# Optimization experiments

Hardware: AMD Instinct MI355X
Metric: run time of the kernel (lower is better)

The kernel has to match this reference:

```python
import jax, jax.numpy as jnp
import numpy as np

B, S, D = 4, 2048, 1024
H, DK, DV = 16, 64, 64
SCALE = 8.0  # scaling_factor = sqrt(dk)


def setup_inputs() -> dict:
    key = jax.random.key(0)
    ks = jax.random.split(key, 9)
    s = 1.0 / np.sqrt(D)
    return {
        "q": jax.random.normal(ks[0], (B, S, D), jnp.float32),
        "k": jax.random.normal(ks[1], (B, S, D), jnp.float32),
        "v": jax.random.normal(ks[2], (B, S, D), jnp.float32),
        "Wq": jax.random.uniform(ks[3], (D, H * DK), jnp.float32, -s, s),
        "bq": jax.random.uniform(ks[4], (H * DK,), jnp.float32, -s, s),
        "Wk": jax.random.uniform(ks[5], (D, H * DK), jnp.float32, -s, s),
        "bk": jax.random.uniform(ks[6], (H * DK,), jnp.float32, -s, s),
        "Wv": jax.random.uniform(ks[7], (D, H * DV), jnp.float32, -s, s),
        "bv": jax.random.uniform(ks[8], (H * DV,), jnp.float32, -s, s),
    }


def reference(q, k, v, Wq, bq, Wk, bk, Wv, bv):
    # Linear projections, then split heads: [B,S,H*d] -> [B,S,H,d]
    qh = (q @ Wq + bq).reshape(B, S, H, DK)
    kh = (k @ Wk + bk).reshape(B, S, H, DK)
    vh = (v @ Wv + bv).reshape(B, S, H, DV)
    # scores: [B,H,Sq,Sk]
    e = jnp.einsum("bqhd,bkhd->bhqk", qh, kh) / SCALE
    attn = jax.nn.softmax(e, axis=-1)
    out = jnp.einsum("bhqk,bkhd->bqhd", attn, vh)  # [B,Sq,H,DV]
    return out.reshape(B, S, H * DV)  # dropout p=0 -> identity
```

## Files before the change

### kernel.cpp

```cpp
#include <hip/hip_runtime.h>
#include <hip/hip_bf16.h>


typedef unsigned short u16;
typedef unsigned int   u32;
typedef short bf16x8 __attribute__((ext_vector_type(8)));
typedef short bf16x4 __attribute__((ext_vector_type(4)));
typedef float f32x4  __attribute__((ext_vector_type(4)));
typedef u32   u32x4  __attribute__((ext_vector_type(4)));

#define S_TOT 2048
#define HD    1024
#define QK_SCALE 0.18033688f

#if __has_builtin(__builtin_amdgcn_exp2f)
#define EXP2(x) __builtin_amdgcn_exp2f(x)
#else
#define EXP2(x) exp2f(x)
#endif

__device__ __forceinline__ u16 f2bf(float f) {
  union { float f; unsigned u; } v; v.f = f;
  unsigned r = v.u + 0x7FFFu + ((v.u >> 16) & 1u);
  return (u16)(r >> 16);
}

__device__ __forceinline__ u32 cvt_pk_bf16(float lo, float hi) {
  u32 r;
  asm("v_cvt_pk_bf16_f32 %0, %1, %2" : "=v"(r) : "v"(lo), "v"(hi));
  return r;
}

__device__ __forceinline__ bf16x4 ds_tr16(unsigned a) {
  bf16x4 d;
  asm volatile("ds_read_b64_tr_b16 %0, %1" : "=v"(d) : "v"(a) : "memory");
  return d;
}

__device__ __forceinline__ void gld16(const u16* g, u16* l) {
  __builtin_amdgcn_global_load_lds(
      (const __attribute__((address_space(1))) u32*)g,
      (__attribute__((address_space(3))) u32*)l, 16, 0, 0);
}

#define LGKM_FENCE() do { asm volatile("s_waitcnt lgkmcnt(0)" ::: "memory"); \
                          __builtin_amdgcn_sched_barrier(0); } while (0)

__global__ __launch_bounds__(256)
void conv_kernel(const float* __restrict__ x0, const float* __restrict__ x1, const float* __restrict__ x2,
                 const float* __restrict__ w0, const float* __restrict__ w1, const float* __restrict__ w2,
                 u16* __restrict__ Xb, u16* __restrict__ Wt)
{
  const int z = blockIdx.y;
  const int t = threadIdx.x;
  if (blockIdx.x < 1024) {
    const float* X = z == 0 ? x0 : (z == 1 ? x1 : x2);
    u16* Xz = Xb + (size_t)z * 8388608;
    int tid = blockIdx.x * 256 + t;
#pragma unroll
    for (int i = 0; i < 8; ++i) {
      int c = tid + i * 262144;
      int row = c >> 8, k4 = (c & 255) * 4;
      const float4 xv = *(const float4*)&X[(size_t)row * 1024 + k4];
      int p = (k4 & ~31) + 8 * ((k4 & 15) >> 2) + 4 * ((k4 >> 4) & 1);
      bf16x4 sv = { (short)f2bf(xv.x), (short)f2bf(xv.y), (short)f2bf(xv.z), (short)f2bf(xv.w) };
      *(bf16x4*)&Xz[(size_t)row * 1024 + p] = sv;
    }
  } else {
    const float* W = z == 0 ? w0 : (z == 1 ? w1 : w2);
    u16* Wz = Wt + (size_t)z * 1048576;
    int tid = (blockIdx.x - 1024) * 256 + t;
#pragma unroll
    for (int i = 0; i < 8; ++i) {
      int c = tid + i * 32768;
      int k = c >> 8, n4 = (c & 255) * 4;
      const float4 wv = *(const float4*)&W[(size_t)k * 1024 + n4];
      int off = ((n4 >> 7) * 32 + (k >> 5)) * 4096 + ((n4 >> 4) & 7) * 512
              + ((k >> 4) & 1) * 256 + (k & 15) * 16 + (n4 & 15);
      bf16x4 sv = { (short)f2bf(wv.x), (short)f2bf(wv.y), (short)f2bf(wv.z), (short)f2bf(wv.w) };
      *(bf16x4*)&Wz[off] = sv;
    }
  }
}

__global__ __launch_bounds__(256)
void gemm_kernel(const u16* __restrict__ Xb, const u16* __restrict__ Wt,
                 const float* __restrict__ b0, const float* __restrict__ b1, const float* __restrict__ b2,
                 u16* __restrict__ o0, u16* __restrict__ o1, u16* __restrict__ vT)
{
  int p  = blockIdx.x + 8 * blockIdx.y + 512 * blockIdx.z;
  int wk = (p & 7) * 192 + (p >> 3);
  int nb = wk & 7, mb = (wk >> 3) & 63, z = wk >> 9;

  const u16* Xz = Xb + (size_t)z * 8388608;
  const u16* Wz = Wt + (size_t)z * 1048576;
  const float* BS = z == 0 ? b0 : (z == 1 ? b1 : b2);
  const float  osc = (z == 0) ? QK_SCALE : 1.0f;

  const int t = threadIdx.x;
  const int lane = t & 63, wid = t >> 6;
  const int g = lane >> 4, ln = lane & 15;
  const int mbase = mb * 128, nbase = nb * 128;

  __shared__ __align__(16) u16 Al[128 * 32];
  __shared__ __align__(16) u16 Bl[16 * 256];

  f32x4 acc[4][4];
#pragma unroll
  for (int i = 0; i < 4; ++i)
#pragma unroll
    for (int j = 0; j < 4; ++j) { acc[i][j][0]=0.f; acc[i][j][1]=0.f; acc[i][j][2]=0.f; acc[i][j][3]=0.f; }

  const u16* sa = Xz + (size_t)(mbase + (t >> 2)) * 1024 + (t & 3) * 8;
  const u16* sb = Wz + (size_t)(nb * 32) * 4096 + t * 8;
  u16* al_w = &Al[wid * 512];
  u16* bl_w = &Bl[wid * 512];

  if (z < 2) {
    const int wm = wid >> 1, wn = wid & 1;
    u16* O = z == 0 ? o0 : o1;
    const unsigned bs_base = (unsigned)(size_t)&Bl[0] + (unsigned)((wn * 4) * 1024) + lane * 8;

    for (int kb = 0; kb < 32; ++kb) {
      gld16(sa + kb * 32,                 al_w);
      gld16(sa + kb * 32 + 64 * 1024,     al_w + 2048);
      gld16(sb + kb * 4096,               bl_w);
      gld16(sb + kb * 4096 + 2048,        bl_w + 2048);
      __syncthreads();

      bf16x8 af[4];
#pragma unroll
      for (int mf = 0; mf < 4; ++mf)
        af[mf] = *(const bf16x8*)&Al[(wm * 64 + mf * 16 + ln) * 32 + g * 8];

      bf16x8 bfv[4];
#pragma unroll
      for (int nf = 0; nf < 4; ++nf) {
        bf16x4 lo = ds_tr16(bs_base + (unsigned)(nf * 1024));
        bf16x4 hi = ds_tr16(bs_base + (unsigned)(nf * 1024 + 512));
        bf16x8 bb;
        bb[0]=lo[0]; bb[1]=lo[1]; bb[2]=lo[2]; bb[3]=lo[3];
        bb[4]=hi[0]; bb[5]=hi[1]; bb[6]=hi[2]; bb[7]=hi[3];
        bfv[nf] = bb;
      }
      LGKM_FENCE();
#pragma unroll
      for (int mf = 0; mf < 4; ++mf)
#pragma unroll
        for (int nf = 0; nf < 4; ++nf)
          acc[mf][nf] = __builtin_amdgcn_mfma_f32_16x16x32_bf16(af[mf], bfv[nf], acc[mf][nf], 0, 0, 0);
      __syncthreads();
    }

#pragma unroll
    for (int nf = 0; nf < 4; ++nf) {
      int n = nbase + wn * 64 + nf * 16 + ln;
      float bv = BS[n];
#pragma unroll
      for (int mf = 0; mf < 4; ++mf)
#pragma unroll
        for (int r = 0; r < 4; ++r) {
          int m = mbase + wm * 64 + mf * 16 + 4 * g + r;
          O[(size_t)m * 1024 + n] = f2bf((acc[mf][nf][r] + bv) * osc);
        }
    }
  } else {
    const int wseq = wid >> 1, wdv = wid & 1;
    const unsigned bs_base2 = (unsigned)(size_t)&Bl[0] + (unsigned)((wdv * 4) * 1024) + lane * 8;

    for (int kb = 0; kb < 32; ++kb) {
      gld16(sa + kb * 32,                 al_w);
      gld16(sa + kb * 32 + 64 * 1024,     al_w + 2048);
      gld16(sb + kb * 4096,               bl_w);
      gld16(sb + kb * 4096 + 2048,        bl_w + 2048);
      __syncthreads();

      bf16x8 afw[4];
#pragma unroll
      for (int mf = 0; mf < 4; ++mf) {
        bf16x4 lo = ds_tr16(bs_base2 + (unsigned)(mf * 1024));
        bf16x4 hi = ds_tr16(bs_base2 + (unsigned)(mf * 1024 + 512));
        bf16x8 bb;
        bb[0]=lo[0]; bb[1]=lo[1]; bb[2]=lo[2]; bb[3]=lo[3];
        bb[4]=hi[0]; bb[5]=hi[1]; bb[6]=hi[2]; bb[7]=hi[3];
        afw[mf] = bb;
      }
      bf16x8 bfx[4];
#pragma unroll
      for (int nf = 0; nf < 4; ++nf)
        bfx[nf] = *(const bf16x8*)&Al[(wseq * 64 + nf * 16 + ln) * 32 + g * 8];
      LGKM_FENCE();
#pragma unroll
      for (int mf = 0; mf < 4; ++mf)
#pragma unroll
        for (int nf = 0; nf < 4; ++nf)
          acc[mf][nf] = __builtin_amdgcn_mfma_f32_16x16x32_bf16(afw[mf], bfx[nf], acc[mf][nf], 0, 0, 0);
      __syncthreads();
    }

#pragma unroll
    for (int mf = 0; mf < 4; ++mf)
#pragma unroll
      for (int r = 0; r < 4; ++r) {
        int dvg = nbase + wdv * 64 + mf * 16 + 4 * g + r;
        float bv = BS[dvg];
        int hh = dvg >> 6, dvl = dvg & 63;
#pragma unroll
        for (int nf = 0; nf < 4; ++nf) {
          int m = mbase + wseq * 64 + nf * 16 + ln;
          int bb = m >> 11, ss = m & 2047;
          vT[((size_t)(bb * 16 + hh) * 64 + dvl) * 2048 + ss] = f2bf(acc[mf][nf][r] + bv);
        }
      }
  }
}

__global__ __launch_bounds__(256)
void proj_kernel(const float* __restrict__ x0, const float* __restrict__ x1, const float* __restrict__ x2,
                 const float* __restrict__ w0, const float* __restrict__ w1, const float* __restrict__ w2,
                 const float* __restrict__ b0, const float* __restrict__ b1, const float* __restrict__ b2,
                 u16* __restrict__ o0, u16* __restrict__ o1, u16* __restrict__ vT)
{
  int p  = blockIdx.x + 8 * blockIdx.y + 512 * blockIdx.z;
  int wk = (p & 7) * 192 + (p >> 3);
  int nb = wk & 7, mb = (wk >> 3) & 63, z = wk >> 9;

  const float* X  = z == 0 ? x0 : (z == 1 ? x1 : x2);
  const float* W  = z == 0 ? w0 : (z == 1 ? w1 : w2);
  const float* BS = z == 0 ? b0 : (z == 1 ? b1 : b2);
  const float  osc = (z == 0) ? QK_SCALE : 1.0f;

  const int t = threadIdx.x;
  const int lane = t & 63, wid = t >> 6;
  const int g = lane >> 4, ln = lane & 15;
  const int wm = wid >> 1, wn = wid & 1;
  const int mbase = mb * 128, nbase = nb * 128;

  __shared__ __align__(16) u16 As[128 * 40];
  __shared__ __align__(16) u16 Bs[16 * 272];

  f32x4 acc[4][4];
#pragma unroll
  for (int i = 0; i < 4; ++i)
#pragma unroll
    for (int j = 0; j < 4; ++j) { acc[i][j][0]=0.f; acc[i][j][1]=0.f; acc[i][j][2]=0.f; acc[i][j][3]=0.f; }

  const int arow = t >> 3;
  const int ak0  = (t & 7) * 4;
  const int ap   = 8 * ((ak0 & 15) >> 2) + 4 * (ak0 >> 4);
  const int bkr  = t >> 5;
  const int bnc  = (t & 31) * 4;
  const int bnblk = bnc >> 4, bncl = bnc & 15;

  const unsigned bs_base = (unsigned)(size_t)&Bs[0];

  for (int kb = 0; kb < 32; ++kb) {
    const int kbase = kb * 32;
#pragma unroll
    for (int ps = 0; ps < 4; ++ps) {
      int row = arow + 32 * ps;
      const float4 xv = *(const float4*)&X[(size_t)(mbase + row) * 1024 + kbase + ak0];
      bf16x4 sv = { (short)f2bf(xv.x), (short)f2bf(xv.y), (short)f2bf(xv.z), (short)f2bf(xv.w) };
      *(bf16x4*)&As[row * 40 + ap] = sv;
    }
#pragma unroll
    for (int ps = 0; ps < 4; ++ps) {
      int kr = bkr + 8 * ps;
      const float4 wv = *(const float4*)&W[(size_t)(kbase + kr) * 1024 + nbase + bnc];
      bf16x4 sv = { (short)f2bf(wv.x), (short)f2bf(wv.y), (short)f2bf(wv.z), (short)f2bf(wv.w) };
      *(bf16x4*)&Bs[(bnblk * 2 + (kr >> 4)) * 272 + (kr & 15) * 16 + bncl] = sv;
    }
    __syncthreads();

    bf16x8 af[4];
#pragma unroll
    for (int mf = 0; mf < 4; ++mf)
      af[mf] = *(const bf16x8*)&As[(wm * 64 + mf * 16 + ln) * 40 + g * 8];

    bf16x8 bfv[4];
#pragma unroll
    for (int nf = 0; nf < 4; ++nf) {
      unsigned base = bs_base + (unsigned)(((wn * 4 + nf) * 2) * 544) + lane * 8;
      bf16x4 lo = ds_tr16(base);
      bf16x4 hi = ds_tr16(base + 544);
      bf16x8 bb;
      bb[0]=lo[0]; bb[1]=lo[1]; bb[2]=lo[2]; bb[3]=lo[3];
      bb[4]=hi[0]; bb[5]=hi[1]; bb[6]=hi[2]; bb[7]=hi[3];
      bfv[nf] = bb;
    }
    LGKM_FENCE();
#pragma unroll
    for (int mf = 0; mf < 4; ++mf)
#pragma unroll
      for (int nf = 0; nf < 4; ++nf)
        acc[mf][nf] = __builtin_amdgcn_mfma_f32_16x16x32_bf16(af[mf], bfv[nf], acc[mf][nf], 0, 0, 0);
    __syncthreads();
  }

#pragma unroll
  for (int nf = 0; nf < 4; ++nf) {
    int n = nbase + wn * 64 + nf * 16 + ln;
    float bv = BS[n];
#pragma unroll
    for (int mf = 0; mf < 4; ++mf)
#pragma unroll
      for (int r = 0; r < 4; ++r) {
        int m = mbase + wm * 64 + mf * 16 + 4 * g + r;
        float val = (acc[mf][nf][r] + bv) * osc;
        if (z < 2) {
          u16* O = z == 0 ? o0 : o1;
          O[(size_t)m * 1024 + n] = f2bf(val);
        } else {
          vT[((size_t)((m >> 11) * 16 + (n >> 6)) * 64 + (n & 63)) * 2048 + (m & 2047)] = f2bf(val);
        }
      }
  }
}

__global__ __launch_bounds__(512)
void attn_kernel(const u16* __restrict__ qh, const u16* __restrict__ kh, const u16* __restrict__ vT,
                 float* __restrict__ out)
{
  int p  = blockIdx.x + 8 * blockIdx.y + 128 * blockIdx.z;
  int wk = (p & 7) * 64 + (p >> 3);
  int qt = wk & 7, h = (wk >> 3) & 15, b = wk >> 7;

  const int t = threadIdx.x;
  const int lane = t & 63, wid = t >> 6;
  const int g = lane >> 4, ln = lane & 15;
  const size_t bS = (size_t)b * S_TOT;
  const int qwin = qt * 256 + wid * 32;

  __shared__ __align__(16) u16 Ks[64 * 72];
  __shared__ __align__(16) u16 Vt[64 * 72];

  bf16x8 qf[2][2];
#pragma unroll
  for (int nf = 0; nf < 2; ++nf) {
    const u16* qrow = &qh[(bS + qwin + nf * 16 + ln) * HD + h * 64];
#pragma unroll
    for (int kk = 0; kk < 2; ++kk) {
      bf16x4 lo = *(const bf16x4*)&qrow[kk * 32 + 4 * g];
      bf16x4 hi = *(const bf16x4*)&qrow[kk * 32 + 4 * g + 16];
      bf16x8 qq;
      qq[0]=lo[0]; qq[1]=lo[1]; qq[2]=lo[2]; qq[3]=lo[3];
      qq[4]=hi[0]; qq[5]=hi[1]; qq[6]=hi[2]; qq[7]=hi[3];
      qf[nf][kk] = qq;
    }
  }

  bf16x8 ones;
#pragma unroll
  for (int j = 0; j < 8; ++j) ones[j] = (short)0x3F80;

  f32x4 o[2][4];
#pragma unroll
  for (int i = 0; i < 2; ++i)
#pragma unroll
    for (int j = 0; j < 4; ++j) { o[i][j][0]=0.f; o[i][j][1]=0.f; o[i][j][2]=0.f; o[i][j][3]=0.f; }
  f32x4 o1[2];
  o1[0][0]=0.f; o1[0][1]=0.f; o1[0][2]=0.f; o1[0][3]=0.f;
  o1[1][0]=0.f; o1[1][1]=0.f; o1[1][2]=0.f; o1[1][3]=0.f;

  const int skv = t >> 4;
  const int sd0 = (t & 15) * 4;
  const int kpos = 32 * (sd0 >> 5) + 8 * ((sd0 & 15) >> 2) + 4 * ((sd0 >> 4) & 1);
  u16* ksw[2];
  ksw[0] = &Ks[skv * 72 + kpos];
  ksw[1] = &Ks[(skv + 32) * 72 + kpos];
  const u16* kp = &kh[(bS + skv) * HD + h * 64 + sd0];

  const int vdv  = t >> 3;
  const int vkv8 = (t & 7) * 8;
  const int vp0  = 32 * (vkv8 >> 5) + 8 * ((vkv8 & 15) >> 2) + 4 * ((vkv8 >> 4) & 1);
  const int vkv4 = vkv8 + 4;
  const int vp1  = 32 * (vkv4 >> 5) + 8 * ((vkv4 & 15) >> 2) + 4 * ((vkv4 >> 4) & 1);
  u16* vsw0 = &Vt[vdv * 72 + vp0];
  u16* vsw1 = &Vt[vdv * 72 + vp1];
  const u16* vp = &vT[((size_t)(b * 16 + h) * 64 + vdv) * 2048 + vkv8];

  const size_t KSTEP = (size_t)64 * HD, C32 = (size_t)32 * HD;

  bf16x4 kr[2];
  kr[0] = *(const bf16x4*)kp; kr[1] = *(const bf16x4*)(kp + C32);
  bf16x8 vr = *(const bf16x8*)vp;
  kp += KSTEP; vp += 64;

  for (int it = 0; it < 32; ++it) {
    *(bf16x4*)ksw[0] = kr[0];
    *(bf16x4*)ksw[1] = kr[1];
    bf16x4 vlo = { vr[0], vr[1], vr[2], vr[3] };
    bf16x4 vhi = { vr[4], vr[5], vr[6], vr[7] };
    *(bf16x4*)vsw0 = vlo;
    *(bf16x4*)vsw1 = vhi;
    __syncthreads();

    if (it < 31) {
      kr[0] = *(const bf16x4*)kp; kr[1] = *(const bf16x4*)(kp + C32);
      vr = *(const bf16x8*)vp;
      kp += KSTEP; vp += 64;
    }

#pragma unroll
    for (int s = 0; s < 2; ++s) {
      bf16x8 kf[2][2];
#pragma unroll
      for (int mf = 0; mf < 2; ++mf)
#pragma unroll
        for (int kk = 0; kk < 2; ++kk)
          kf[mf][kk] = *(const bf16x8*)&Ks[(s * 32 + mf * 16 + ln) * 72 + kk * 32 + 8 * g];

      f32x4 sc[2][2];
      __builtin_amdgcn_s_setprio(1);
#pragma unroll
      for (int mf = 0; mf < 2; ++mf)
#pragma unroll
        for (int nf = 0; nf < 2; ++nf) {
          f32x4 a; a[0]=0.f; a[1]=0.f; a[2]=0.f; a[3]=0.f;
#pragma unroll
          for (int kk = 0; kk < 2; ++kk)
            a = __builtin_amdgcn_mfma_f32_16x16x32_bf16(kf[mf][kk], qf[nf][kk], a, 0, 0, 0);
          sc[mf][nf] = a;
        }
      __builtin_amdgcn_s_setprio(0);

      bf16x8 vf[4];
#pragma unroll
      for (int nf = 0; nf < 4; ++nf)
        vf[nf] = *(const bf16x8*)&Vt[(nf * 16 + ln) * 72 + s * 32 + 8 * g];

      bf16x8 pa[2];
#pragma unroll
      for (int nf = 0; nf < 2; ++nf) {
        float pv[2][4];
#pragma unroll
        for (int mf = 0; mf < 2; ++mf)
#pragma unroll
          for (int r = 0; r < 4; ++r)
            pv[mf][r] = EXP2(sc[mf][nf][r]);
        union { u32x4 u; bf16x8 b; } pk;
        pk.u[0] = cvt_pk_bf16(pv[0][0], pv[0][1]);
        pk.u[1] = cvt_pk_bf16(pv[0][2], pv[0][3]);
        pk.u[2] = cvt_pk_bf16(pv[1][0], pv[1][1]);
        pk.u[3] = cvt_pk_bf16(pv[1][2], pv[1][3]);
        pa[nf] = pk.b;
      }

      __builtin_amdgcn_s_setprio(1);
#pragma unroll
      for (int mq = 0; mq < 2; ++mq) {
#pragma unroll
        for (int nf = 0; nf < 4; ++nf)
          o[mq][nf] = __builtin_amdgcn_mfma_f32_16x16x32_bf16(pa[mq], vf[nf], o[mq][nf], 0, 0, 0);
        o1[mq] = __builtin_amdgcn_mfma_f32_16x16x32_bf16(pa[mq], ones, o1[mq], 0, 0, 0);
      }
      __builtin_amdgcn_s_setprio(0);
    }
    __syncthreads();
  }

#pragma unroll
  for (int mq = 0; mq < 2; ++mq)
#pragma unroll
    for (int r = 0; r < 4; ++r) {
      float inv = 1.0f / o1[mq][r];
      int qrow = qwin + mq * 16 + 4 * g + r;
#pragma unroll
      for (int nf = 0; nf < 4; ++nf)
        out[(bS + qrow) * HD + h * 64 + nf * 16 + ln] = o[mq][nf][r] * inv;
    }
}

extern "C" void kernel_launch(void* const* d_in, const int* in_sizes, int n_in,
                              void* d_out, int out_size, void* d_ws, size_t ws_size,
                              hipStream_t stream) {
  const float* q  = (const float*)d_in[0];
  const float* k  = (const float*)d_in[1];
  const float* v  = (const float*)d_in[2];
  const float* Wq = (const float*)d_in[3];
  const float* bq = (const float*)d_in[4];
  const float* Wk = (const float*)d_in[5];
  const float* bk = (const float*)d_in[6];
  const float* Wv = (const float*)d_in[7];
  const float* bv = (const float*)d_in[8];
  float* out = (float*)d_out;

  u16* qh = (u16*)d_ws;
  u16* kh = qh + (size_t)8192 * 1024;
  u16* vT = kh + (size_t)8192 * 1024;

  const size_t XB_OFF = (size_t)3 * 8192 * 1024;
  const size_t WT_OFF = XB_OFF + (size_t)3 * 8192 * 1024;
  const size_t NEED   = (WT_OFF + (size_t)3 * 1024 * 1024) * 2;

  if (ws_size >= NEED) {
    u16* Xb = (u16*)d_ws + XB_OFF;
    u16* Wt = (u16*)d_ws + WT_OFF;
    conv_kernel<<<dim3(1152, 3), 256, 0, stream>>>(q, k, v, Wq, Wk, Wv, Xb, Wt);
    gemm_kernel<<<dim3(8, 64, 3), 256, 0, stream>>>(Xb, Wt, bq, bk, bv, qh, kh, vT);
  } else {
    proj_kernel<<<dim3(8, 64, 3), 256, 0, stream>>>(q, k, v, Wq, Wk, Wv, bq, bk, bv, qh, kh, vT);
  }
  attn_kernel<<<dim3(8, 16, 4), 512, 0, stream>>>(qh, kh, vT, out);
}
```

Measured before the change: 178.6 us.

## Double-buffer LDS tiles in projection GEMM to overlap loads with MFMA

The projection GEMM's shared-memory A and B tiles become two buffers. The main loop now issues the global-to-LDS loads for the next k-block before computing on the current one, so memory latency overlaps with the matrix math instead of being exposed behind each barrier. The MFMA sections are also wrapped in s_setprio raises to favour issuing the math waves. The cost is twice the LDS footprint, which may lower occupancy, and the loop still relies on __syncthreads to wait for the async loads.

```diff
diff --git a/kernel.cpp b/kernel.cpp
--- a/kernel.cpp
+++ b/kernel.cpp
@@ -102,8 +102,8 @@
   const int g = lane >> 4, ln = lane & 15;
   const int mbase = mb * 128, nbase = nb * 128;
 
-  __shared__ __align__(16) u16 Al[128 * 32];
-  __shared__ __align__(16) u16 Bl[16 * 256];
+  __shared__ __align__(16) u16 Al[2][128 * 32];
+  __shared__ __align__(16) u16 Bl[2][16 * 256];
 
   f32x4 acc[4][4];
 #pragma unroll
@@ -113,42 +113,57 @@
 
   const u16* sa = Xz + (size_t)(mbase + (t >> 2)) * 1024 + (t & 3) * 8;
   const u16* sb = Wz + (size_t)(nb * 32) * 4096 + t * 8;
-  u16* al_w = &Al[wid * 512];
-  u16* bl_w = &Bl[wid * 512];
+  u16* alw[2] = { &Al[0][wid * 512], &Al[1][wid * 512] };
+  u16* blw[2] = { &Bl[0][wid * 512], &Bl[1][wid * 512] };
+
+  auto stage = [&](int kb, int buf) __attribute__((always_inline)) {
+    gld16(sa + kb * 32,               alw[buf]);
+    gld16(sa + kb * 32 + 64 * 1024,   alw[buf] + 2048);
+    gld16(sb + kb * 4096,             blw[buf]);
+    gld16(sb + kb * 4096 + 2048,      blw[buf] + 2048);
+  };
+
+  stage(0, 0);
+  __syncthreads();
 
   if (z < 2) {
     const int wm = wid >> 1, wn = wid & 1;
     u16* O = z == 0 ? o0 : o1;
-    const unsigned bs_base = (unsigned)(size_t)&Bl[0] + (unsigned)((wn * 4) * 1024) + lane * 8;
-
-    for (int kb = 0; kb < 32; ++kb) {
-      gld16(sa + kb * 32,                 al_w);
-      gld16(sa + kb * 32 + 64 * 1024,     al_w + 2048);
-      gld16(sb + kb * 4096,               bl_w);
-      gld16(sb + kb * 4096 + 2048,        bl_w + 2048);
-      __syncthreads();
-
+    const unsigned bsb[2] = {
+      (unsigned)(size_t)&Bl[0][0] + (unsigned)((wn * 4) * 1024) + lane * 8,
+      (unsigned)(size_t)&Bl[1][0] + (unsigned)((wn * 4) * 1024) + lane * 8 };
+
+    auto compute = [&](int cur) __attribute__((always_inline)) {
       bf16x8 af[4];
 #pragma unroll
       for (int mf = 0; mf < 4; ++mf)
-        af[mf] = *(const bf16x8*)&Al[(wm * 64 + mf * 16 + ln) * 32 + g * 8];
-
+        af[mf] = *(const bf16x8*)&Al[cur][(wm * 64 + mf * 16 + ln) * 32 + g * 8];
       bf16x8 bfv[4];
 #pragma unroll
       for (int nf = 0; nf < 4; ++nf) {
-        bf16x4 lo = ds_tr16(bs_base + (unsigned)(nf * 1024));
-        bf16x4 hi = ds_tr16(bs_base + (unsigned)(nf * 1024 + 512));
+        bf16x4 lo = ds_tr16(bsb[cur] + (unsigned)(nf * 1024));
+        bf16x4 hi = ds_tr16(bsb[cur] + (unsigned)(nf * 1024 + 512));
         bf16x8 bb;
         bb[0]=lo[0]; bb[1]=lo[1]; bb[2]=lo[2]; bb[3]=lo[3];
         bb[4]=hi[0]; bb[5]=hi[1]; bb[6]=hi[2]; bb[7]=hi[3];
         bfv[nf] = bb;
       }
       LGKM_FENCE();
+      __builtin_amdgcn_s_setprio(1);
 #pragma unroll
       for (int mf = 0; mf < 4; ++mf)
 #pragma unroll
         for (int nf = 0; nf < 4; ++nf)
           acc[mf][nf] = __builtin_amdgcn_mfma_f32_16x16x32_bf16(af[mf], bfv[nf], acc[mf][nf], 0, 0, 0);
+      __builtin_amdgcn_s_setprio(0);
+    };
+
+    for (int kb = 0; kb < 32; kb += 2) {
+      if (kb + 1 < 32) stage(kb + 1, 1);
+      compute(0);
+      __syncthreads();
+      if (kb + 2 < 32) stage(kb + 2, 0);
+      compute(1);
       __syncthreads();
     }
 
@@ -166,20 +181,16 @@
     }
   } else {
     const int wseq = wid >> 1, wdv = wid & 1;
-    const unsigned bs_base2 = (unsigned)(size_t)&Bl[0] + (unsigned)((wdv * 4) * 1024) + lane * 8;
-
-    for (int kb = 0; kb < 32; ++kb) {
-      gld16(sa + kb * 32,                 al_w);
-      gld16(sa + kb * 32 + 64 * 1024,     al_w + 2048);
-      gld16(sb + kb * 4096,               bl_w);
-      gld16(sb + kb * 4096 + 2048,        bl_w + 2048);
-      __syncthreads();
-
+    const unsigned bsb2[2] = {
+      (unsigned)(size_t)&Bl[0][0] + (unsigned)((wdv * 4) * 1024) + lane * 8,
+      (unsigned)(size_t)&Bl[1][0] + (unsigned)((wdv * 4) * 1024) + lane * 8 };
+
+    auto compute2 = [&](int cur) __attribute__((always_inline)) {
       bf16x8 afw[4];
 #pragma unroll
       for (int mf = 0; mf < 4; ++mf) {
-        bf16x4 lo = ds_tr16(bs_base2 + (unsigned)(mf * 1024));
-        bf16x4 hi = ds_tr16(bs_base2 + (unsigned)(mf * 1024 + 512));
+        bf16x4 lo = ds_tr16(bsb2[cur] + (unsigned)(mf * 1024));
+        bf16x4 hi = ds_tr16(bsb2[cur] + (unsigned)(mf * 1024 + 512));
         bf16x8 bb;
         bb[0]=lo[0]; bb[1]=lo[1]; bb[2]=lo[2]; bb[3]=lo[3];
         bb[4]=hi[0]; bb[5]=hi[1]; bb[6]=hi[2]; bb[7]=hi[3];
@@ -188,13 +199,23 @@
       bf16x8 bfx[4];
 #pragma unroll
       for (int nf = 0; nf < 4; ++nf)
-        bfx[nf] = *(const bf16x8*)&Al[(wseq * 64 + nf * 16 + ln) * 32 + g * 8];
+        bfx[nf] = *(const bf16x8*)&Al[cur][(wseq * 64 + nf * 16 + ln) * 32 + g * 8];
       LGKM_FENCE();
+      __builtin_amdgcn_s_setprio(1);
 #pragma unroll
       for (int mf = 0; mf < 4; ++mf)
 #pragma unroll
         for (int nf = 0; nf < 4; ++nf)
           acc[mf][nf] = __builtin_amdgcn_mfma_f32_16x16x32_bf16(afw[mf], bfx[nf], acc[mf][nf], 0, 0, 0);
+      __builtin_amdgcn_s_setprio(0);
+    };
+
+    for (int kb = 0; kb < 32; kb += 2) {
+      if (kb + 1 < 32) stage(kb + 1, 1);
+      compute2(0);
+      __syncthreads();
+      if (kb + 2 < 32) stage(kb + 2, 0);
+      compute2(1);
       __syncthreads();
     }
 
```

After: 171.8 us. 1.04x faster.
